# Optimization experiments

Measured on AMD Instinct MI355X. Metric: run time of the kernel, lower is better.

Reference implementation:

```python
import jax, jax.numpy as jnp
import numpy as np

# Model dims
B, S, D = 2, 1024, 1024          # batch, seq, d_model
NH, HD = 16, 64                  # n_heads, head_dim
E, K, H = 8, 2, 4096             # num_experts, experts_per_token, expert hidden
EPS = 1e-6
ROPE_BASE = 10000.0


def rmsnorm(x, w):
    # RMSNorm: x * rsqrt(mean(x^2) + eps) * weight (no mean-centering, no bias)
    return x * jax.lax.rsqrt(jnp.mean(x * x, axis=-1, keepdims=True) + EPS) * w


def apply_rope(q, k):
    # q,k: [B, NH, S, HD]; position_ids = arange(S) broadcast over batch
    hd = q.shape[-1]
    s = q.shape[2]
    inv_freq = 1.0 / (ROPE_BASE ** (jnp.arange(0, hd, 2, dtype=jnp.float32) / hd))
    freqs = jnp.arange(s, dtype=jnp.float32)[:, None] * inv_freq          # [S, HD/2]
    emb = jnp.concatenate([freqs, freqs], axis=-1)                        # [S, HD]
    cos = jnp.cos(emb)[None, None]                                        # [1,1,S,HD]
    sin = jnp.sin(emb)[None, None]

    def rotate_half(x):
        x1, x2 = jnp.split(x, 2, axis=-1)
        return jnp.concatenate([-x2, x1], axis=-1)

    return q * cos + rotate_half(q) * sin, k * cos + rotate_half(k) * sin


def setup_inputs() -> dict:
    key = jax.random.key(0)
    ks = jax.random.split(key, 9)
    sc = 0.02
    return {
        "x": jax.random.normal(ks[0], (B, S, D), jnp.float32),
        "attn_norm_w": jnp.ones((D,), jnp.float32),
        "wq": jax.random.normal(ks[1], (D, D), jnp.float32) * sc,
        "wk": jax.random.normal(ks[2], (D, D), jnp.float32) * sc,
        "wv": jax.random.normal(ks[3], (D, D), jnp.float32) * sc,
        "wo": jax.random.normal(ks[4], (D, D), jnp.float32) * sc,
        "moe_norm_w": jnp.ones((D,), jnp.float32),
        "gate_w": jax.random.normal(ks[5], (E, D), jnp.float32) * sc,
        "w1": jax.random.normal(ks[6], (E, H, D), jnp.float32) * sc,
        "b1": jnp.zeros((E, H), jnp.float32),
        "w2": jax.random.normal(ks[7], (E, D, H), jnp.float32) * sc,
        "b2": jnp.zeros((E, D), jnp.float32),
    }


def reference(x, attn_norm_w, wq, wk, wv, wo, moe_norm_w, gate_w, w1, b1, w2, b2):
    b, s, d = x.shape
    # --- pre-norm causal self-attention with RoPE (eval mode: no dropout) ---
    t = rmsnorm(x, attn_norm_w)
    q = (t @ wq.T).reshape(b, s, NH, HD).transpose(0, 2, 1, 3)
    k = (t @ wk.T).reshape(b, s, NH, HD).transpose(0, 2, 1, 3)
    v = (t @ wv.T).reshape(b, s, NH, HD).transpose(0, 2, 1, 3)
    q, k = apply_rope(q, k)
    scores = jnp.einsum("bhqd,bhkd->bhqk", q, k) / np.float32(np.sqrt(HD))
    causal = jnp.tril(jnp.ones((s, s), bool))
    scores = jnp.where(causal, scores, jnp.float32(-1e30))
    attn = jax.nn.softmax(scores, axis=-1)
    ao = jnp.einsum("bhqk,bhkd->bhqd", attn, v).transpose(0, 2, 1, 3).reshape(b, s, d)
    h = x + ao @ wo.T

    # --- sparse top-k MoE FFN (internal RMSNorm + residual) ---
    tn = rmsnorm(h, moe_norm_w).reshape(-1, d)                  # [T, D]
    logits = tn @ gate_w.T                                      # [T, E]
    gate_scores, idx = jax.lax.top_k(logits, K)                 # [T, K]
    rw = jax.nn.softmax(gate_scores, axis=-1)                   # [T, K]
    # compute all experts densely, then gather selected (same math as
    # gathering per-token expert weight matrices, far less memory traffic)
    hid = jax.nn.gelu(jnp.einsum("td,ehd->teh", tn, w1) + b1, approximate=False)
    eo = jnp.einsum("teh,edh->ted", hid, w2) + b2               # [T, E, D]
    sel = jnp.take_along_axis(eo, idx[:, :, None], axis=1)      # [T, K, D]
    moe_out = jnp.einsum("tkd,tk->td", sel, rw).reshape(b, s, d)
    return h + moe_out
```

## Files before the change

kernel.cpp:

```cpp
#include <hip/hip_runtime.h>
#include <hip/hip_bf16.h>
#include <hip/hip_fp16.h>


#define T_TOK 2048
#define DMODEL 1024
#define SEQ 1024
#define NEXP 8
#define HEXP 4096

typedef __attribute__((ext_vector_type(4))) float f32x4;
typedef __attribute__((ext_vector_type(4))) int i32x4;
typedef __attribute__((ext_vector_type(8))) short short8;
typedef __attribute__((ext_vector_type(8))) _Float16 half8;
typedef __attribute__((ext_vector_type(4))) _Float16 half4;

#define WAIT_VM3 asm volatile("s_waitcnt vmcnt(3)" ::: "memory")
#define WAIT_VM4 asm volatile("s_waitcnt vmcnt(4)" ::: "memory")
#define WAIT_VM6 asm volatile("s_waitcnt vmcnt(6)" ::: "memory")
#define WAIT_VM0 asm volatile("s_waitcnt vmcnt(0)" ::: "memory")
#define BARRIER __builtin_amdgcn_s_barrier()
#define SCHEDFENCE __builtin_amdgcn_sched_barrier(0)

__device__ __forceinline__ void gload16(const void* g, void* l)
{
    __builtin_amdgcn_global_load_lds((const __attribute__((address_space(1))) void*)g,
                                     (__attribute__((address_space(3))) void*)l, 16, 0, 0);
}

__device__ __forceinline__ void bsplit(float f, unsigned short& hi, unsigned short& lo)
{
    unsigned int u = __float_as_uint(f);
    unsigned int rh = (u + 0x7FFFu + ((u >> 16) & 1u)) >> 16;
    hi = (unsigned short)rh;
    float fl = f - __uint_as_float(rh << 16);
    unsigned int u2 = __float_as_uint(fl);
    lo = (unsigned short)((u2 + 0x7FFFu + ((u2 >> 16) & 1u)) >> 16);
}

__device__ __forceinline__ float gelu_fast(float v)
{
    float e = __expf(-1.5957691216f * v * (1.0f + 0.044715f * v * v));
    return v * __builtin_amdgcn_rcpf(1.0f + e);
}

__global__ __launch_bounds__(256) void cast2_f16_kernel(
    const float* __restrict__ s0, const float* __restrict__ s1,
    _Float16* __restrict__ d0, _Float16* __restrict__ d1, int n8)
{
    const float* src = blockIdx.y ? s1 : s0;
    _Float16* dst = blockIdx.y ? d1 : d0;
    int stride = gridDim.x * blockDim.x;
    for (int i = blockIdx.x * blockDim.x + threadIdx.x; i < n8; i += stride) {
        float4 a = ((const float4*)src)[2 * i];
        float4 b = ((const float4*)src)[2 * i + 1];
        half8 h = { (_Float16)a.x, (_Float16)a.y, (_Float16)a.z, (_Float16)a.w,
                    (_Float16)b.x, (_Float16)b.y, (_Float16)b.z, (_Float16)b.w };
        *(half8*)(dst + (size_t)i * 8) = h;
    }
}

__global__ __launch_bounds__(256) void split4_kernel(
    const float* __restrict__ s0, const float* __restrict__ s1,
    const float* __restrict__ s2, const float* __restrict__ s3,
    unsigned short* __restrict__ h0, unsigned short* __restrict__ h1,
    unsigned short* __restrict__ h2, unsigned short* __restrict__ h3,
    unsigned short* __restrict__ l0, unsigned short* __restrict__ l1,
    unsigned short* __restrict__ l2, unsigned short* __restrict__ l3, int n4)
{
    int z = blockIdx.y;
    const float* src = (z == 0) ? s0 : (z == 1) ? s1 : (z == 2) ? s2 : s3;
    unsigned short* hi = (z == 0) ? h0 : (z == 1) ? h1 : (z == 2) ? h2 : h3;
    unsigned short* lo = (z == 0) ? l0 : (z == 1) ? l1 : (z == 2) ? l2 : l3;
    int stride = gridDim.x * blockDim.x;
    for (int i = blockIdx.x * blockDim.x + threadIdx.x; i < n4; i += stride) {
        float4 v = ((const float4*)src)[i];
        ushort4 h, l;
        bsplit(v.x, h.x, l.x); bsplit(v.y, h.y, l.y);
        bsplit(v.z, h.z, l.z); bsplit(v.w, h.w, l.w);
        *(ushort4*)(hi + (size_t)i * 4) = h;
        *(ushort4*)(lo + (size_t)i * 4) = l;
    }
}

__global__ __launch_bounds__(256) void rmsnorm_kernel(const float* __restrict__ x,
                                                      const float* __restrict__ w,
                                                      float* __restrict__ of,
                                                      _Float16* __restrict__ oh,
                                                      unsigned short* __restrict__ ohi,
                                                      unsigned short* __restrict__ olo)
{
    int row = blockIdx.x;
    int t = threadIdx.x;
    float4 v = ((const float4*)(x + (size_t)row * DMODEL))[t];
    float ss = v.x * v.x + v.y * v.y + v.z * v.z + v.w * v.w;
#pragma unroll
    for (int off = 32; off > 0; off >>= 1) ss += __shfl_xor(ss, off);
    __shared__ float red[4];
    if ((t & 63) == 0) red[t >> 6] = ss;
    __syncthreads();
    float tot = red[0] + red[1] + red[2] + red[3];
    float sc = rsqrtf(tot * (1.0f / DMODEL) + 1e-6f);
    float4 w4 = ((const float4*)w)[t];
    float4 o;
    o.x = v.x * sc * w4.x; o.y = v.y * sc * w4.y; o.z = v.z * sc * w4.z; o.w = v.w * sc * w4.w;
    if (of) ((float4*)(of + (size_t)row * DMODEL))[t] = o;
    if (oh) {
        half4 h = { (_Float16)o.x, (_Float16)o.y, (_Float16)o.z, (_Float16)o.w };
        *(half4*)(oh + (size_t)row * DMODEL + t * 4) = h;
    }
    if (ohi) {
        ushort4 h, l;
        bsplit(o.x, h.x, l.x); bsplit(o.y, h.y, l.y);
        bsplit(o.z, h.z, l.z); bsplit(o.w, h.w, l.w);
        *(ushort4*)(ohi + (size_t)row * DMODEL + t * 4) = h;
        *(ushort4*)(olo + (size_t)row * DMODEL + t * 4) = l;
    }
}

__global__ __launch_bounds__(256) void gemm_split_kernel(
    const unsigned short* __restrict__ aH, const unsigned short* __restrict__ aL,
    const unsigned short* __restrict__ b0H, const unsigned short* __restrict__ b0L,
    const unsigned short* __restrict__ b1H, const unsigned short* __restrict__ b1L,
    const unsigned short* __restrict__ b2H, const unsigned short* __restrict__ b2L,
    float* __restrict__ C0, float* __restrict__ C1, float* __restrict__ C2,
    const float* __restrict__ resid, int K)
{
    const unsigned short* bH = (blockIdx.z == 0) ? b0H : (blockIdx.z == 1 ? b1H : b2H);
    const unsigned short* bL = (blockIdx.z == 0) ? b0L : (blockIdx.z == 1 ? b1L : b2L);
    float* C = (blockIdx.z == 0) ? C0 : (blockIdx.z == 1 ? C1 : C2);
    int m0 = blockIdx.y * 128, n0 = blockIdx.x * 64;
    __shared__ unsigned short AsH[2][128 * 32];
    __shared__ unsigned short AsL[2][128 * 32];
    __shared__ unsigned short BsH[2][64 * 32];
    __shared__ unsigned short BsL[2][64 * 32];
    int t = threadIdx.x, w = t >> 6, l = t & 63;
    int sa = l >> 2, sc = (l & 3) * 8;
    const unsigned short* gAH0 = aH + (size_t)(m0 + w * 32 + sa) * K + sc;
    const unsigned short* gAH1 = aH + (size_t)(m0 + w * 32 + 16 + sa) * K + sc;
    const unsigned short* gAL0 = aL + (size_t)(m0 + w * 32 + sa) * K + sc;
    const unsigned short* gAL1 = aL + (size_t)(m0 + w * 32 + 16 + sa) * K + sc;
    const unsigned short* gBH0 = bH + (size_t)(n0 + w * 16 + sa) * K + sc;
    const unsigned short* gBL0 = bL + (size_t)(n0 + w * 16 + sa) * K + sc;
    const int aoff0 = (w * 32) * 32;
    const int aoff1 = (w * 32 + 16) * 32;
    const int boff0 = (w * 16) * 32;
    int wr = w >> 1, wc = w & 1;
    f32x4 zero = { 0.0f, 0.0f, 0.0f, 0.0f };
    f32x4 acc[4][2];
#pragma unroll
    for (int i = 0; i < 4; i++)
#pragma unroll
        for (int j = 0; j < 2; j++) acc[i][j] = zero;

#define GS_STAGE(B, K0) do { \
    gload16(gAH0 + (K0), &AsH[B][aoff0]); gload16(gAH1 + (K0), &AsH[B][aoff1]); \
    gload16(gAL0 + (K0), &AsL[B][aoff0]); gload16(gAL1 + (K0), &AsL[B][aoff1]); \
    gload16(gBH0 + (K0), &BsH[B][boff0]); gload16(gBL0 + (K0), &BsL[B][boff0]); \
} while (0)

#define GS_COMPUTE(B) do { \
    short8 ah[4], al[4], bh8[2], bl8[2]; \
    _Pragma("unroll") \
    for (int mi = 0; mi < 4; mi++) { \
        int base = (wr * 64 + mi * 16 + (l & 15)) * 32 + (l >> 4) * 8; \
        ah[mi] = *(const short8*)&AsH[B][base]; \
        al[mi] = *(const short8*)&AsL[B][base]; } \
    _Pragma("unroll") \
    for (int ni = 0; ni < 2; ni++) { \
        int base = (wc * 32 + ni * 16 + (l & 15)) * 32 + (l >> 4) * 8; \
        bh8[ni] = *(const short8*)&BsH[B][base]; \
        bl8[ni] = *(const short8*)&BsL[B][base]; } \
    _Pragma("unroll") \
    for (int mi = 0; mi < 4; mi++) \
        _Pragma("unroll") \
        for (int ni = 0; ni < 2; ni++) { \
            acc[mi][ni] = __builtin_amdgcn_mfma_f32_16x16x32_bf16(ah[mi], bh8[ni], acc[mi][ni], 0, 0, 0); \
            acc[mi][ni] = __builtin_amdgcn_mfma_f32_16x16x32_bf16(ah[mi], bl8[ni], acc[mi][ni], 0, 0, 0); \
            acc[mi][ni] = __builtin_amdgcn_mfma_f32_16x16x32_bf16(al[mi], bh8[ni], acc[mi][ni], 0, 0, 0); } \
} while (0)

    const int nt = K >> 5;
    GS_STAGE(0, 0);
    for (int kt = 0; kt < nt; kt += 2) {
        GS_STAGE(1, (kt + 1) << 5);
        WAIT_VM6;
        BARRIER; SCHEDFENCE;
        GS_COMPUTE(0);
        BARRIER;
        if (kt + 2 < nt) {
            GS_STAGE(0, (kt + 2) << 5);
            WAIT_VM6;
        } else {
            WAIT_VM0;
        }
        BARRIER; SCHEDFENCE;
        GS_COMPUTE(1);
        BARRIER;
    }
#undef GS_STAGE
#undef GS_COMPUTE

#pragma unroll
    for (int mi = 0; mi < 4; mi++) {
#pragma unroll
        for (int r = 0; r < 4; r++) {
            int row = m0 + wr * 64 + mi * 16 + (l >> 4) * 4 + r;
#pragma unroll
            for (int ni = 0; ni < 2; ni++) {
                int col = n0 + wc * 32 + ni * 16 + (l & 15);
                float v = acc[mi][ni][r];
                if (resid) v += resid[(size_t)row * DMODEL + col];
                C[(size_t)row * DMODEL + col] = v;
            }
        }
    }
}

__global__ __launch_bounds__(256) void rope_split_kernel(
    const float* __restrict__ qf, const float* __restrict__ kf,
    unsigned short* __restrict__ qHi, unsigned short* __restrict__ qLo,
    unsigned short* __restrict__ kHi, unsigned short* __restrict__ kLo)
{
    int i = blockIdx.x * 256 + threadIdx.x;
    int tok = i >> 9;
    int r = i & 511;
    int hh = r >> 5, ii = r & 31;
    int s = tok & (SEQ - 1);
    int b = tok >> 10;
    float invf = powf(10000.0f, -(float)(2 * ii) * (1.0f / 64.0f));
    float ang = (float)s * invf;
    float c = cosf(ang), sn = sinf(ang);
    size_t base = (size_t)tok * DMODEL + hh * 64 + ii;
    float q1 = qf[base], q2 = qf[base + 32];
    float k1 = kf[base], k2 = kf[base + 32];
    float rq1 = (q1 * c - q2 * sn) * 0.125f;
    float rq2 = (q2 * c + q1 * sn) * 0.125f;
    float rk1 = k1 * c - k2 * sn;
    float rk2 = k2 * c + k1 * sn;
    int bh = b * 16 + hh;
    size_t qb = ((size_t)bh * SEQ + s) * 64 + ii;
    unsigned short h, lo;
    bsplit(rq1, h, lo); qHi[qb] = h; qLo[qb] = lo;
    bsplit(rq2, h, lo); qHi[qb + 32] = h; qLo[qb + 32] = lo;
    size_t kb = (size_t)bh * (SEQ * 64) + (size_t)(s >> 6) * 4096 + (size_t)(s & 63) * 64;
    int d1 = ii, d2 = ii + 32;
    int p1 = (((d1 >> 3) ^ (s & 7)) << 3) | (d1 & 7);
    int p2 = (((d2 >> 3) ^ (s & 7)) << 3) | (d2 & 7);
    bsplit(rk1, h, lo); kHi[kb + p1] = h; kLo[kb + p1] = lo;
    bsplit(rk2, h, lo); kHi[kb + p2] = h; kLo[kb + p2] = lo;
}

__global__ __launch_bounds__(256) void vtrans_kernel(const float* __restrict__ vf,
                                                     unsigned short* __restrict__ vtHi,
                                                     unsigned short* __restrict__ vtLo)
{
    int sb = blockIdx.x, bh = blockIdx.y;
    int b = bh >> 4, h = bh & 15;
    __shared__ unsigned short tH[64][72];
    __shared__ unsigned short tL[64][72];
    int t = threadIdx.x;
#pragma unroll
    for (int i = 0; i < 4; i++) {
        int idx = i * 256 + t, row = idx >> 4, c4 = idx & 15;
        float4 v = *(const float4*)(vf + (size_t)(b * SEQ + sb * 64 + row) * DMODEL + h * 64 + c4 * 4);
        unsigned short hh, ll;
        bsplit(v.x, hh, ll); tH[c4 * 4 + 0][row] = hh; tL[c4 * 4 + 0][row] = ll;
        bsplit(v.y, hh, ll); tH[c4 * 4 + 1][row] = hh; tL[c4 * 4 + 1][row] = ll;
        bsplit(v.z, hh, ll); tH[c4 * 4 + 2][row] = hh; tL[c4 * 4 + 2][row] = ll;
        bsplit(v.w, hh, ll); tH[c4 * 4 + 3][row] = hh; tL[c4 * 4 + 3][row] = ll;
    }
    __syncthreads();
#pragma unroll
    for (int i = 0; i < 4; i++) {
        int idx = i * 256 + t, d = idx >> 4, sc4 = idx & 15;
        ushort4 oh = { tH[d][sc4 * 4 + 0], tH[d][sc4 * 4 + 1], tH[d][sc4 * 4 + 2], tH[d][sc4 * 4 + 3] };
        ushort4 ol = { tL[d][sc4 * 4 + 0], tL[d][sc4 * 4 + 1], tL[d][sc4 * 4 + 2], tL[d][sc4 * 4 + 3] };
        size_t off = (size_t)bh * (64 * SEQ) + (size_t)sb * 4096 + (size_t)d * 64
                   + (((sc4 >> 1) ^ (d & 7)) << 3) + ((sc4 & 1) << 2);
        *(ushort4*)(vtHi + off) = oh;
        *(ushort4*)(vtLo + off) = ol;
    }
}

__global__ __launch_bounds__(512) void attn_mfma_kernel(
    const unsigned short* __restrict__ qHi, const unsigned short* __restrict__ qLo,
    const unsigned short* __restrict__ kHi, const unsigned short* __restrict__ kLo,
    const unsigned short* __restrict__ vtHi, const unsigned short* __restrict__ vtLo,
    float* __restrict__ Opart, float* __restrict__ mscr, float* __restrict__ lscr)
{
    int qt = 7 - blockIdx.x;
    int bh = blockIdx.y, ks = blockIdx.z;
    int t = threadIdx.x, w = t >> 6, l = t & 63;
    int lq = l & 15, g = l >> 4, lx = lq & 7;
    __shared__ unsigned short KsH[2][4096];
    __shared__ unsigned short KsL[2][4096];
    __shared__ unsigned short VsH[2][4096];
    __shared__ unsigned short VsL[2][4096];
    __shared__ unsigned short PsH[8][1024];
    __shared__ unsigned short PsL[8][1024];
    const size_t hb = (size_t)bh * (SEQ * 64);
    const unsigned short* kHp = kHi + hb;
    const unsigned short* kLp = kLo + hb;
    const unsigned short* vHp = vtHi + hb;
    const unsigned short* vLp = vtLo + hb;
    int qrow = qt * 128 + w * 16 + lq;
    short8 qh[2], qlo8[2];
#pragma unroll
    for (int c = 0; c < 2; c++) {
        size_t off = hb + (size_t)qrow * 64 + c * 32 + g * 8;
        qh[c]   = *(const short8*)(qHi + off);
        qlo8[c] = *(const short8*)(qLo + off);
    }
    f32x4 zero = { 0.0f, 0.0f, 0.0f, 0.0f };
    f32x4 acc_o[4];
#pragma unroll
    for (int i = 0; i < 4; i++) acc_o[i] = zero;
    float mrun = -3.0e38f, lrun = 0.0f;
    int ktl = ks ? (qt + 1) : 0;
    int kth = ks ? (2 * qt + 2) : (qt + 1);

#define AT_STAGE(B, KT) do { \
    size_t so = (size_t)(KT) * 4096 + (w * 64 + l) * 8; \
    gload16(kHp + so, &KsH[B][w * 512]); \
    gload16(kLp + so, &KsL[B][w * 512]); \
    gload16(vHp + so, &VsH[B][w * 512]); \
    gload16(vLp + so, &VsL[B][w * 512]); \
} while (0)

#define AT_COMPUTE(B, KT) do { \
    f32x4 sacc[4]; \
    _Pragma("unroll") \
    for (int i = 0; i < 4; i++) sacc[i] = zero; \
    _Pragma("unroll") \
    for (int nf = 0; nf < 4; nf++) { \
        _Pragma("unroll") \
        for (int c = 0; c < 2; c++) { \
            int ka = (nf * 16 + lq) * 64 + (((c * 4 + g) ^ lx) << 3); \
            short8 kh = *(const short8*)&KsH[B][ka]; \
            short8 kl = *(const short8*)&KsL[B][ka]; \
            sacc[nf] = __builtin_amdgcn_mfma_f32_16x16x32_bf16(kh, qh[c], sacc[nf], 0, 0, 0); \
            sacc[nf] = __builtin_amdgcn_mfma_f32_16x16x32_bf16(kh, qlo8[c], sacc[nf], 0, 0, 0); \
            sacc[nf] = __builtin_amdgcn_mfma_f32_16x16x32_bf16(kl, qh[c], sacc[nf], 0, 0, 0); \
        } \
    } \
    _Pragma("unroll") \
    for (int nf = 0; nf < 4; nf++) \
        _Pragma("unroll") \
        for (int r = 0; r < 4; r++) \
            if ((KT) * 64 + nf * 16 + g * 4 + r > qrow) sacc[nf][r] = -1.0e30f; \
    float mt = sacc[0][0]; \
    _Pragma("unroll") \
    for (int nf = 0; nf < 4; nf++) \
        _Pragma("unroll") \
        for (int r = 0; r < 4; r++) mt = fmaxf(mt, sacc[nf][r]); \
    mt = fmaxf(mt, __shfl_xor(mt, 16)); \
    mt = fmaxf(mt, __shfl_xor(mt, 32)); \
    float mnew = fmaxf(mrun, mt); \
    float p[4][4]; \
    float ps = 0.0f; \
    _Pragma("unroll") \
    for (int nf = 0; nf < 4; nf++) \
        _Pragma("unroll") \
        for (int r = 0; r < 4; r++) { \
            float e = __expf(sacc[nf][r] - mnew); \
            p[nf][r] = e; \
            ps += e; \
        } \
    ps += __shfl_xor(ps, 16); \
    ps += __shfl_xor(ps, 32); \
    float scale = __expf(mrun - mnew); \
    lrun = lrun * scale + ps; \
    mrun = mnew; \
    _Pragma("unroll") \
    for (int nf = 0; nf < 4; nf++) { \
        ushort4 ph, pl; \
        bsplit(p[nf][0], ph.x, pl.x); bsplit(p[nf][1], ph.y, pl.y); \
        bsplit(p[nf][2], ph.z, pl.z); bsplit(p[nf][3], ph.w, pl.w); \
        int pa = lq * 64 + (((nf * 2 + (g >> 1)) ^ lx) << 3) + ((g & 1) << 2); \
        *(ushort4*)&PsH[w][pa] = ph; \
        *(ushort4*)&PsL[w][pa] = pl; \
    } \
    float scq[4]; \
    _Pragma("unroll") \
    for (int r = 0; r < 4; r++) scq[r] = __shfl(scale, g * 4 + r); \
    _Pragma("unroll") \
    for (int df = 0; df < 4; df++) \
        _Pragma("unroll") \
        for (int r = 0; r < 4; r++) acc_o[df][r] *= scq[r]; \
    _Pragma("unroll") \
    for (int c = 0; c < 2; c++) { \
        int pa = lq * 64 + (((c * 4 + g) ^ lx) << 3); \
        short8 ph8 = *(const short8*)&PsH[w][pa]; \
        short8 pl8 = *(const short8*)&PsL[w][pa]; \
        _Pragma("unroll") \
        for (int df = 0; df < 4; df++) { \
            int va = (df * 16 + lq) * 64 + (((c * 4 + g) ^ lx) << 3); \
            short8 vh = *(const short8*)&VsH[B][va]; \
            short8 vl = *(const short8*)&VsL[B][va]; \
            acc_o[df] = __builtin_amdgcn_mfma_f32_16x16x32_bf16(ph8, vh, acc_o[df], 0, 0, 0); \
            acc_o[df] = __builtin_amdgcn_mfma_f32_16x16x32_bf16(ph8, vl, acc_o[df], 0, 0, 0); \
            acc_o[df] = __builtin_amdgcn_mfma_f32_16x16x32_bf16(pl8, vh, acc_o[df], 0, 0, 0); \
        } \
    } \
} while (0)

    int kt = ktl;
    AT_STAGE(0, kt);
    for (; kt + 1 < kth; kt += 2) {
        AT_STAGE(1, kt + 1);
        WAIT_VM4;
        BARRIER; SCHEDFENCE;
        AT_COMPUTE(0, kt);
        BARRIER;
        if (kt + 2 < kth) {
            AT_STAGE(0, kt + 2);
            WAIT_VM4;
        } else {
            WAIT_VM0;
        }
        BARRIER; SCHEDFENCE;
        AT_COMPUTE(1, kt + 1);
        BARRIER;
    }
    if (kt < kth) {
        WAIT_VM0;
        BARRIER; SCHEDFENCE;
        AT_COMPUTE(0, kt);
    }
#undef AT_STAGE
#undef AT_COMPUTE

    if (g == 0) {
        size_t mi = (size_t)(ks * 32 + bh) * SEQ + (size_t)(qt * 128 + w * 16 + lq);
        mscr[mi] = mrun;
        lscr[mi] = lrun;
    }
#pragma unroll
    for (int df = 0; df < 4; df++)
#pragma unroll
        for (int r = 0; r < 4; r++) {
            size_t row = (size_t)(ks * 32 + bh) * SEQ + (size_t)(qt * 128 + w * 16 + g * 4 + r);
            Opart[row * 64 + df * 16 + lq] = acc_o[df][r];
        }
}

__global__ __launch_bounds__(256) void attn_combine_kernel(
    const float* __restrict__ Opart, const float* __restrict__ mscr,
    const float* __restrict__ lscr,
    unsigned short* __restrict__ aoHi, unsigned short* __restrict__ aoLo)
{
    int i = blockIdx.x * 256 + threadIdx.x;
    int d4 = i & 15;
    int qr = (i >> 4) & (SEQ - 1);
    int bh = i >> 14;
    int b = bh >> 4, h = bh & 15;
    size_t r0 = (size_t)bh * SEQ + qr;
    size_t r1 = (size_t)(32 + bh) * SEQ + qr;
    float m0 = mscr[r0], m1 = mscr[r1];
    float l0 = lscr[r0], l1 = lscr[r1];
    float m = fmaxf(m0, m1);
    float w0 = __expf(m0 - m), w1 = __expf(m1 - m);
    float dn = 1.0f / (w0 * l0 + w1 * l1);
    float4 o0 = *(const float4*)(Opart + r0 * 64 + d4 * 4);
    float4 o1 = *(const float4*)(Opart + r1 * 64 + d4 * 4);
    float4 o;
    o.x = (w0 * o0.x + w1 * o1.x) * dn;
    o.y = (w0 * o0.y + w1 * o1.y) * dn;
    o.z = (w0 * o0.z + w1 * o1.z) * dn;
    o.w = (w0 * o0.w + w1 * o1.w) * dn;
    ushort4 hs, ls;
    bsplit(o.x, hs.x, ls.x); bsplit(o.y, hs.y, ls.y);
    bsplit(o.z, hs.z, ls.z); bsplit(o.w, hs.w, ls.w);
    size_t base = (size_t)b * SEQ * DMODEL + (size_t)qr * DMODEL + h * 64 + d4 * 4;
    *(ushort4*)(aoHi + base) = hs;
    *(ushort4*)(aoLo + base) = ls;
}

__global__ __launch_bounds__(256) void gate_kernel(const float* __restrict__ tn2f,
                                                   const float* __restrict__ gw,
                                                   float* __restrict__ logits)
{
    int tok = blockIdx.x;
    int t = threadIdx.x, e = t >> 5, l32 = t & 31;
    const float* xr = tn2f + (size_t)tok * DMODEL;
    const float* gr = gw + (size_t)e * DMODEL;
    float s = 0.0f;
    for (int j = l32; j < DMODEL; j += 32) s += xr[j] * gr[j];
#pragma unroll
    for (int off = 16; off > 0; off >>= 1) s += __shfl_down(s, off, 32);
    if (l32 == 0) logits[tok * NEXP + e] = s;
}

__global__ void zero_kernel(int* p, int n)
{
    int i = blockIdx.x * blockDim.x + threadIdx.x;
    if (i < n) p[i] = 0;
}

__global__ void top2_kernel(const float* __restrict__ logits, float* __restrict__ rw,
                            int* __restrict__ cnt, int* __restrict__ entry)
{
    int t = blockIdx.x * blockDim.x + threadIdx.x;
    if (t >= T_TOK) return;
    float l[8];
#pragma unroll
    for (int e = 0; e < 8; e++) l[e] = logits[t * 8 + e];
    int e0 = 0;
#pragma unroll
    for (int e = 1; e < 8; e++) if (l[e] > l[e0]) e0 = e;
    int e1 = (e0 == 0) ? 1 : 0;
#pragma unroll
    for (int e = 0; e < 8; e++) if (e != e0 && l[e] > l[e1]) e1 = e;
    float ex = expf(l[e1] - l[e0]);
    float denom = 1.0f + ex;
    rw[t * 2 + 0] = 1.0f / denom;
    rw[t * 2 + 1] = ex / denom;
    int pos = atomicAdd(&cnt[e0], 1);
    entry[e0 * 2048 + pos] = t * 2;
    pos = atomicAdd(&cnt[e1], 1);
    entry[e1 * 2048 + pos] = t * 2 + 1;
}

__global__ void offs_kernel(const int* __restrict__ cnt, int* __restrict__ offs)
{
    if (threadIdx.x == 0) {
        int s = 0;
        for (int e = 0; e < 8; e++) { offs[e] = s; s += cnt[e]; }
    }
}

__global__ __launch_bounds__(256) void moe_gemm1_kernel(
    const _Float16* __restrict__ tn2h, const _Float16* __restrict__ w1h,
    const float* __restrict__ b1, const int* __restrict__ cnt, const int* __restrict__ offs,
    const int* __restrict__ entry, _Float16* __restrict__ hid)
{
    int e = blockIdx.z;
    int ne = cnt[e];
    int m0 = blockIdx.y * 128;
    if (m0 >= ne) return;
    int n0 = blockIdx.x * 128;
    __shared__ _Float16 As[2][128 * 32];
    __shared__ _Float16 Bs[2][128 * 32];
    int t = threadIdx.x, w = t >> 6, l = t & 63;
    int sa = l >> 2, sc = (l & 3) * 8;
    int g0 = entry[e * 2048 + min(m0 + w * 32 + sa, ne - 1)] >> 1;
    int g1 = entry[e * 2048 + min(m0 + w * 32 + 16 + sa, ne - 1)] >> 1;
    const _Float16* gA0 = tn2h + (size_t)g0 * DMODEL + sc;
    const _Float16* gA1 = tn2h + (size_t)g1 * DMODEL + sc;
    const _Float16* w1e = w1h + (size_t)e * HEXP * DMODEL;
    const _Float16* gB0 = w1e + (size_t)(n0 + w * 32 + sa) * DMODEL + sc;
    const _Float16* gB1 = w1e + (size_t)(n0 + w * 32 + 16 + sa) * DMODEL + sc;
    const int aoff0 = (w * 32) * 32, aoff1 = (w * 32 + 16) * 32;
    int wr = w >> 1, wc = w & 1;
    f32x4 zero = { 0.0f, 0.0f, 0.0f, 0.0f };
    f32x4 acc[4][4];
#pragma unroll
    for (int i = 0; i < 4; i++)
#pragma unroll
        for (int j = 0; j < 4; j++) acc[i][j] = zero;

#define M1_STAGE(B, K0) do { \
    gload16(gA0 + (K0), &As[B][aoff0]); gload16(gA1 + (K0), &As[B][aoff1]); \
    gload16(gB0 + (K0), &Bs[B][aoff0]); gload16(gB1 + (K0), &Bs[B][aoff1]); \
} while (0)

#define M1_COMPUTE(B) do { \
    half8 af[4], bfr[4]; \
    _Pragma("unroll") \
    for (int mi = 0; mi < 4; mi++) \
        af[mi] = *(const half8*)&As[B][(wr * 64 + mi * 16 + (l & 15)) * 32 + (l >> 4) * 8]; \
    _Pragma("unroll") \
    for (int ni = 0; ni < 4; ni++) \
        bfr[ni] = *(const half8*)&Bs[B][(wc * 64 + ni * 16 + (l & 15)) * 32 + (l >> 4) * 8]; \
    _Pragma("unroll") \
    for (int mi = 0; mi < 4; mi++) \
        _Pragma("unroll") \
        for (int ni = 0; ni < 4; ni++) \
            acc[mi][ni] = __builtin_amdgcn_mfma_f32_16x16x32_f16(af[mi], bfr[ni], acc[mi][ni], 0, 0, 0); \
} while (0)

    const int nt = DMODEL >> 5;
    M1_STAGE(0, 0);
    for (int kt = 0; kt < nt; kt += 2) {
        M1_STAGE(1, (kt + 1) << 5);
        WAIT_VM4;
        BARRIER; SCHEDFENCE;
        M1_COMPUTE(0);
        BARRIER;
        if (kt + 2 < nt) {
            M1_STAGE(0, (kt + 2) << 5);
            WAIT_VM4;
        } else {
            WAIT_VM0;
        }
        BARRIER; SCHEDFENCE;
        M1_COMPUTE(1);
        BARRIER;
    }
#undef M1_STAGE
#undef M1_COMPUTE

    int off_e = offs[e];
#pragma unroll
    for (int mi = 0; mi < 4; mi++) {
#pragma unroll
        for (int r = 0; r < 4; r++) {
            int row = m0 + wr * 64 + mi * 16 + (l >> 4) * 4 + r;
            if (row < ne) {
                size_t orow = (size_t)(off_e + row) * HEXP;
#pragma unroll
                for (int ni = 0; ni < 4; ni++) {
                    int cg = n0 + wc * 64 + ni * 16 + (l & 15);
                    float v = acc[mi][ni][r] + b1[e * HEXP + cg];
                    hid[orow + cg] = (_Float16)gelu_fast(v);
                }
            }
        }
    }
}

__global__ __launch_bounds__(512) void moe_gemm2_kernel(
    const _Float16* __restrict__ hid, const _Float16* __restrict__ w2h,
    const float* __restrict__ b2, const int* __restrict__ cnt, const int* __restrict__ offs,
    const int* __restrict__ entry,
    float* __restrict__ eoA, float* __restrict__ eoB,
    float* __restrict__ eoC, float* __restrict__ eoD)
{
    int bid = blockIdx.x;
    int e = bid & 7;
    int rest = bid >> 3;
    int n_i = rest & 7;
    int rest2 = rest >> 3;
    int ks = rest2 & 3;
    int m_i = rest2 >> 2;
    int ne = cnt[e];
    int m0 = m_i * 256;
    if (m0 >= ne) return;
    int n0 = n_i * 128;
    int kbase = ks * (HEXP / 4);
    float* eoP = (ks == 0) ? eoA : (ks == 1) ? eoB : (ks == 2) ? eoC : eoD;
    __shared__ _Float16 As[2][256 * 32];
    __shared__ _Float16 Bs[2][128 * 32];
    int t = threadIdx.x, w = t >> 6, l = t & 63;
    int off_e = offs[e];
    int sa = l >> 2, sc = (l & 3) * 8;
    int r0 = off_e + min(m0 + w * 32 + sa, ne - 1);
    int r1 = off_e + min(m0 + w * 32 + 16 + sa, ne - 1);
    const _Float16* gA0 = hid + (size_t)r0 * HEXP + kbase + sc;
    const _Float16* gA1 = hid + (size_t)r1 * HEXP + kbase + sc;
    const _Float16* w2e = w2h + (size_t)e * DMODEL * HEXP;
    const _Float16* gB0 = w2e + (size_t)(n0 + w * 16 + sa) * HEXP + kbase + sc;
    const int aoff0 = (w * 32) * 32, aoff1 = (w * 32 + 16) * 32;
    const int boff0 = (w * 16) * 32;
    int wr = w >> 1, wc = w & 1;
    f32x4 zero = { 0.0f, 0.0f, 0.0f, 0.0f };
    f32x4 acc[4][4];
#pragma unroll
    for (int i = 0; i < 4; i++)
#pragma unroll
        for (int j = 0; j < 4; j++) acc[i][j] = zero;

#define M2_STAGE(B, K0) do { \
    gload16(gA0 + (K0), &As[B][aoff0]); gload16(gA1 + (K0), &As[B][aoff1]); \
    gload16(gB0 + (K0), &Bs[B][boff0]); \
} while (0)

#define M2_COMPUTE(B) do { \
    half8 af[4], bfr[4]; \
    _Pragma("unroll") \
    for (int mi = 0; mi < 4; mi++) \
        af[mi] = *(const half8*)&As[B][(wr * 64 + mi * 16 + (l & 15)) * 32 + (l >> 4) * 8]; \
    _Pragma("unroll") \
    for (int ni = 0; ni < 4; ni++) \
        bfr[ni] = *(const half8*)&Bs[B][(wc * 64 + ni * 16 + (l & 15)) * 32 + (l >> 4) * 8]; \
    _Pragma("unroll") \
    for (int mi = 0; mi < 4; mi++) \
        _Pragma("unroll") \
        for (int ni = 0; ni < 4; ni++) \
            acc[mi][ni] = __builtin_amdgcn_mfma_f32_16x16x32_f16(af[mi], bfr[ni], acc[mi][ni], 0, 0, 0); \
} while (0)

    const int nt = (HEXP / 4) >> 5;
    M2_STAGE(0, 0);
    for (int kt = 0; kt < nt; kt += 2) {
        M2_STAGE(1, (kt + 1) << 5);
        WAIT_VM3;
        BARRIER; SCHEDFENCE;
        M2_COMPUTE(0);
        BARRIER;
        if (kt + 2 < nt) {
            M2_STAGE(0, (kt + 2) << 5);
            WAIT_VM3;
        } else {
            WAIT_VM0;
        }
        BARRIER; SCHEDFENCE;
        M2_COMPUTE(1);
        BARRIER;
    }
#undef M2_STAGE
#undef M2_COMPUTE

#pragma unroll
    for (int mi = 0; mi < 4; mi++) {
#pragma unroll
        for (int r = 0; r < 4; r++) {
            int row = m0 + wr * 64 + mi * 16 + (l >> 4) * 4 + r;
            if (row < ne) {
                int t2k = entry[e * 2048 + row];
#pragma unroll
                for (int ni = 0; ni < 4; ni++) {
                    int cg = n0 + wc * 64 + ni * 16 + (l & 15);
                    float v = acc[mi][ni][r];
                    if (ks == 0) v += b2[e * DMODEL + cg];
                    eoP[(size_t)t2k * DMODEL + cg] = v;
                }
            }
        }
    }
}

__global__ __launch_bounds__(256) void combine_kernel(const float* __restrict__ hf,
                                                      const float* __restrict__ eoA,
                                                      const float* __restrict__ eoB,
                                                      const float* __restrict__ eoC,
                                                      const float* __restrict__ eoD,
                                                      const float* __restrict__ rw,
                                                      float* __restrict__ out)
{
    int i = blockIdx.x * 256 + threadIdx.x;
    int tok = i >> 8;
    int d4 = i & 255;
    float4 hv = ((const float4*)hf)[i];
    float p0 = rw[tok * 2], p1 = rw[tok * 2 + 1];
    size_t i0 = (size_t)(tok * 2) * 256 + d4;
    size_t i1 = (size_t)(tok * 2 + 1) * 256 + d4;
    float4 a0 = ((const float4*)eoA)[i0];
    float4 b0 = ((const float4*)eoB)[i0];
    float4 c0 = ((const float4*)eoC)[i0];
    float4 d0 = ((const float4*)eoD)[i0];
    float4 a1 = ((const float4*)eoA)[i1];
    float4 b1 = ((const float4*)eoB)[i1];
    float4 c1 = ((const float4*)eoC)[i1];
    float4 d1 = ((const float4*)eoD)[i1];
    float4 o;
    o.x = hv.x + p0 * (a0.x + b0.x + c0.x + d0.x) + p1 * (a1.x + b1.x + c1.x + d1.x);
    o.y = hv.y + p0 * (a0.y + b0.y + c0.y + d0.y) + p1 * (a1.y + b1.y + c1.y + d1.y);
    o.z = hv.z + p0 * (a0.z + b0.z + c0.z + d0.z) + p1 * (a1.z + b1.z + c1.z + d1.z);
    o.w = hv.w + p0 * (a0.w + b0.w + c0.w + d0.w) + p1 * (a1.w + b1.w + c1.w + d1.w);
    ((float4*)out)[i] = o;
}

extern "C" void kernel_launch(void* const* d_in, const int* in_sizes, int n_in,
                              void* d_out, int out_size, void* d_ws, size_t ws_size,
                              hipStream_t stream)
{
    const float* x   = (const float*)d_in[0];
    const float* anw = (const float*)d_in[1];
    const float* wq  = (const float*)d_in[2];
    const float* wk  = (const float*)d_in[3];
    const float* wv  = (const float*)d_in[4];
    const float* wo  = (const float*)d_in[5];
    const float* mnw = (const float*)d_in[6];
    const float* gw  = (const float*)d_in[7];
    const float* w1  = (const float*)d_in[8];
    const float* b1  = (const float*)d_in[9];
    const float* w2  = (const float*)d_in[10];
    const float* b2  = (const float*)d_in[11];
    float* out = (float*)d_out;

    char* p = (char*)d_ws;
    auto alloc = [&](size_t bytes) { char* q = p; p += (bytes + 255) & ~(size_t)255; return q; };
    const size_t TD = (size_t)T_TOK * DMODEL;
    unsigned short* tnHi = (unsigned short*)alloc(TD * 2);
    unsigned short* tnLo = (unsigned short*)alloc(TD * 2);
    float*    qf   = (float*)alloc(TD * 4);
    float*    kf   = (float*)alloc(TD * 4);
    float*    vf   = (float*)alloc(TD * 4);
    unsigned short* qHi = (unsigned short*)alloc(TD * 2);
    unsigned short* qLo = (unsigned short*)alloc(TD * 2);
    unsigned short* kHi = (unsigned short*)alloc(TD * 2);
    unsigned short* kLo = (unsigned short*)alloc(TD * 2);
    float*    hf   = (float*)alloc(TD * 4);
    unsigned short* wqH = (unsigned short*)alloc((size_t)DMODEL * DMODEL * 2);
    unsigned short* wqL = (unsigned short*)alloc((size_t)DMODEL * DMODEL * 2);
    unsigned short* wkH = (unsigned short*)alloc((size_t)DMODEL * DMODEL * 2);
    unsigned short* wkL = (unsigned short*)alloc((size_t)DMODEL * DMODEL * 2);
    unsigned short* wvH = (unsigned short*)alloc((size_t)DMODEL * DMODEL * 2);
    unsigned short* wvL = (unsigned short*)alloc((size_t)DMODEL * DMODEL * 2);
    unsigned short* woH = (unsigned short*)alloc((size_t)DMODEL * DMODEL * 2);
    unsigned short* woL = (unsigned short*)alloc((size_t)DMODEL * DMODEL * 2);
    _Float16* w1h  = (_Float16*)alloc((size_t)NEXP * HEXP * DMODEL * 2);
    _Float16* w2h  = (_Float16*)alloc((size_t)NEXP * HEXP * DMODEL * 2);
    _Float16* hid  = (_Float16*)alloc((size_t)4096 * HEXP * 2);
    float*    logits = (float*)alloc((size_t)T_TOK * NEXP * 4);
    float*    rw   = (float*)alloc((size_t)T_TOK * 2 * 4);
    int*      cnt  = (int*)alloc(256);
    int*      offs = (int*)alloc(256);
    int*      entry = (int*)alloc((size_t)NEXP * 2048 * 4);
    float*    mscr = (float*)alloc((size_t)2 * 32 * SEQ * 4);
    float*    lscr = (float*)alloc((size_t)2 * 32 * SEQ * 4);
    (void)ws_size; (void)in_sizes; (void)n_in; (void)out_size;

    unsigned short* vtHi = (unsigned short*)qf;
    unsigned short* vtLo = (unsigned short*)qf + TD;
    float* tn2f = qf;
    unsigned short* aoHi = (unsigned short*)kf;
    unsigned short* aoLo = (unsigned short*)kf + TD;
    _Float16* tn2h = (_Float16*)vf;
    float* eoA = (float*)qHi;
    float* eoB = (float*)wqH;
    float* Opart = (float*)w1h;
    float* eoC = (float*)((char*)w1h + (size_t)32 * 1024 * 1024);
    float* eoD = (float*)((char*)w1h + (size_t)48 * 1024 * 1024);

    split4_kernel<<<dim3(512, 4), 256, 0, stream>>>(wq, wk, wv, wo,
        wqH, wkH, wvH, woH, wqL, wkL, wvL, woL, DMODEL * DMODEL / 4);

    rmsnorm_kernel<<<T_TOK, 256, 0, stream>>>(x, anw, nullptr, (_Float16*)nullptr, tnHi, tnLo);
    gemm_split_kernel<<<dim3(16, 16, 3), 256, 0, stream>>>(
        tnHi, tnLo, wqH, wqL, wkH, wkL, wvH, wvL, qf, kf, vf, nullptr, DMODEL);
    rope_split_kernel<<<4096, 256, 0, stream>>>(qf, kf, qHi, qLo, kHi, kLo);
    vtrans_kernel<<<dim3(16, 32), 256, 0, stream>>>(vf, vtHi, vtLo);
    attn_mfma_kernel<<<dim3(8, 32, 2), 512, 0, stream>>>(qHi, qLo, kHi, kLo, vtHi, vtLo,
                                                         Opart, mscr, lscr);
    attn_combine_kernel<<<2048, 256, 0, stream>>>(Opart, mscr, lscr, aoHi, aoLo);
    gemm_split_kernel<<<dim3(16, 16, 1), 256, 0, stream>>>(
        aoHi, aoLo, woH, woL, woH, woL, woH, woL, hf, hf, hf, x, DMODEL);

    cast2_f16_kernel<<<dim3(4096, 2), 256, 0, stream>>>(w1, w2, w1h, w2h,
                                                        NEXP * HEXP * DMODEL / 8);

    rmsnorm_kernel<<<T_TOK, 256, 0, stream>>>(hf, mnw, tn2f, tn2h, nullptr, nullptr);
    gate_kernel<<<T_TOK, 256, 0, stream>>>(tn2f, gw, logits);
    zero_kernel<<<1, 64, 0, stream>>>(cnt, 8);
    top2_kernel<<<8, 256, 0, stream>>>(logits, rw, cnt, entry);
    offs_kernel<<<1, 1, 0, stream>>>(cnt, offs);
    moe_gemm1_kernel<<<dim3(32, 16, 8), 256, 0, stream>>>(tn2h, w1h, b1, cnt, offs, entry, hid);
    moe_gemm2_kernel<<<2048, 512, 0, stream>>>(hid, w2h, b2, cnt, offs, entry,
                                               eoA, eoB, eoC, eoD);
    combine_kernel<<<2048, 256, 0, stream>>>(hf, eoA, eoB, eoC, eoD, rw, out);
}
```

Measured before the change: 428.5 us.

## Fuse expert weight cast into attention launch and retile MoE GEMM1 with swizzled LDS

```diff
diff --git a/kernel.cpp b/kernel.cpp
--- a/kernel.cpp
+++ b/kernel.cpp
@@ -42,22 +42,6 @@
 {
     float e = __expf(-1.5957691216f * v * (1.0f + 0.044715f * v * v));
     return v * __builtin_amdgcn_rcpf(1.0f + e);
-}
-
-__global__ __launch_bounds__(256) void cast2_f16_kernel(
-    const float* __restrict__ s0, const float* __restrict__ s1,
-    _Float16* __restrict__ d0, _Float16* __restrict__ d1, int n8)
-{
-    const float* src = blockIdx.y ? s1 : s0;
-    _Float16* dst = blockIdx.y ? d1 : d0;
-    int stride = gridDim.x * blockDim.x;
-    for (int i = blockIdx.x * blockDim.x + threadIdx.x; i < n8; i += stride) {
-        float4 a = ((const float4*)src)[2 * i];
-        float4 b = ((const float4*)src)[2 * i + 1];
-        half8 h = { (_Float16)a.x, (_Float16)a.y, (_Float16)a.z, (_Float16)a.w,
-                    (_Float16)b.x, (_Float16)b.y, (_Float16)b.z, (_Float16)b.w };
-        *(half8*)(dst + (size_t)i * 8) = h;
-    }
 }
 
 __global__ __launch_bounds__(256) void split4_kernel(
@@ -283,14 +267,34 @@
     }
 }
 
-__global__ __launch_bounds__(512) void attn_mfma_kernel(
+__global__ __launch_bounds__(512) void attn_cast_kernel(
     const unsigned short* __restrict__ qHi, const unsigned short* __restrict__ qLo,
     const unsigned short* __restrict__ kHi, const unsigned short* __restrict__ kLo,
     const unsigned short* __restrict__ vtHi, const unsigned short* __restrict__ vtLo,
-    float* __restrict__ Opart, float* __restrict__ mscr, float* __restrict__ lscr)
-{
-    int qt = 7 - blockIdx.x;
-    int bh = blockIdx.y, ks = blockIdx.z;
+    float* __restrict__ Opart, float* __restrict__ mscr, float* __restrict__ lscr,
+    const float* __restrict__ w1f, const float* __restrict__ w2f,
+    _Float16* __restrict__ w1h, _Float16* __restrict__ w2h)
+{
+    int bid = blockIdx.x;
+    if (bid >= 512) {
+        int cb = bid - 512;
+        const float* src = w1f;
+        _Float16* dst = w1h;
+        if (cb >= 512) { src = w2f; dst = w2h; cb -= 512; }
+        const int n8 = NEXP * HEXP * DMODEL / 8;
+        const int stride = 512 * 512;
+        for (int i = cb * 512 + threadIdx.x; i < n8; i += stride) {
+            float4 a = ((const float4*)src)[2 * i];
+            float4 b = ((const float4*)src)[2 * i + 1];
+            half8 h = { (_Float16)a.x, (_Float16)a.y, (_Float16)a.z, (_Float16)a.w,
+                        (_Float16)b.x, (_Float16)b.y, (_Float16)b.z, (_Float16)b.w };
+            *(half8*)(dst + (size_t)i * 8) = h;
+        }
+        return;
+    }
+    int qt = 7 - (bid & 7);
+    int bh = (bid >> 3) & 31;
+    int ks = bid >> 8;
     int t = threadIdx.x, w = t >> 6, l = t & 63;
     int lq = l & 15, g = l >> 4, lx = lq & 7;
     __shared__ unsigned short KsH[2][4096];
@@ -530,28 +534,34 @@
     }
 }
 
-__global__ __launch_bounds__(256) void moe_gemm1_kernel(
+__global__ __launch_bounds__(512) void moe_gemm1_kernel(
     const _Float16* __restrict__ tn2h, const _Float16* __restrict__ w1h,
     const float* __restrict__ b1, const int* __restrict__ cnt, const int* __restrict__ offs,
     const int* __restrict__ entry, _Float16* __restrict__ hid)
 {
-    int e = blockIdx.z;
+    int bid = blockIdx.x;
+    int e = bid & 7;
+    int n_i = (bid >> 3) & 31;
+    int m_i = bid >> 8;
     int ne = cnt[e];
-    int m0 = blockIdx.y * 128;
+    int m0 = m_i * 256;
     if (m0 >= ne) return;
-    int n0 = blockIdx.x * 128;
-    __shared__ _Float16 As[2][128 * 32];
+    int n0 = n_i * 128;
+    __shared__ _Float16 As[2][256 * 32];
     __shared__ _Float16 Bs[2][128 * 32];
     int t = threadIdx.x, w = t >> 6, l = t & 63;
-    int sa = l >> 2, sc = (l & 3) * 8;
+    int sa = l >> 2;
+    int swz = (l >> 3) & 3;
+    int scA = ((l & 3) ^ swz) * 8;
+    int rcol = ((l >> 4) ^ ((l >> 1) & 3)) * 8;
     int g0 = entry[e * 2048 + min(m0 + w * 32 + sa, ne - 1)] >> 1;
     int g1 = entry[e * 2048 + min(m0 + w * 32 + 16 + sa, ne - 1)] >> 1;
-    const _Float16* gA0 = tn2h + (size_t)g0 * DMODEL + sc;
-    const _Float16* gA1 = tn2h + (size_t)g1 * DMODEL + sc;
+    const _Float16* gA0 = tn2h + (size_t)g0 * DMODEL + scA;
+    const _Float16* gA1 = tn2h + (size_t)g1 * DMODEL + scA;
     const _Float16* w1e = w1h + (size_t)e * HEXP * DMODEL;
-    const _Float16* gB0 = w1e + (size_t)(n0 + w * 32 + sa) * DMODEL + sc;
-    const _Float16* gB1 = w1e + (size_t)(n0 + w * 32 + 16 + sa) * DMODEL + sc;
+    const _Float16* gB0 = w1e + (size_t)(n0 + w * 16 + sa) * DMODEL + scA;
     const int aoff0 = (w * 32) * 32, aoff1 = (w * 32 + 16) * 32;
+    const int boff0 = (w * 16) * 32;
     int wr = w >> 1, wc = w & 1;
     f32x4 zero = { 0.0f, 0.0f, 0.0f, 0.0f };
     f32x4 acc[4][4];
@@ -562,17 +572,17 @@
 
 #define M1_STAGE(B, K0) do { \
     gload16(gA0 + (K0), &As[B][aoff0]); gload16(gA1 + (K0), &As[B][aoff1]); \
-    gload16(gB0 + (K0), &Bs[B][aoff0]); gload16(gB1 + (K0), &Bs[B][aoff1]); \
+    gload16(gB0 + (K0), &Bs[B][boff0]); \
 } while (0)
 
 #define M1_COMPUTE(B) do { \
     half8 af[4], bfr[4]; \
     _Pragma("unroll") \
     for (int mi = 0; mi < 4; mi++) \
-        af[mi] = *(const half8*)&As[B][(wr * 64 + mi * 16 + (l & 15)) * 32 + (l >> 4) * 8]; \
+        af[mi] = *(const half8*)&As[B][(wr * 64 + mi * 16 + (l & 15)) * 32 + rcol]; \
     _Pragma("unroll") \
     for (int ni = 0; ni < 4; ni++) \
-        bfr[ni] = *(const half8*)&Bs[B][(wc * 64 + ni * 16 + (l & 15)) * 32 + (l >> 4) * 8]; \
+        bfr[ni] = *(const half8*)&Bs[B][(wc * 64 + ni * 16 + (l & 15)) * 32 + rcol]; \
     _Pragma("unroll") \
     for (int mi = 0; mi < 4; mi++) \
         _Pragma("unroll") \
@@ -584,13 +594,13 @@
     M1_STAGE(0, 0);
     for (int kt = 0; kt < nt; kt += 2) {
         M1_STAGE(1, (kt + 1) << 5);
-        WAIT_VM4;
+        WAIT_VM3;
         BARRIER; SCHEDFENCE;
         M1_COMPUTE(0);
         BARRIER;
         if (kt + 2 < nt) {
             M1_STAGE(0, (kt + 2) << 5);
-            WAIT_VM4;
+            WAIT_VM3;
         } else {
             WAIT_VM0;
         }
@@ -644,13 +654,16 @@
     __shared__ _Float16 Bs[2][128 * 32];
     int t = threadIdx.x, w = t >> 6, l = t & 63;
     int off_e = offs[e];
-    int sa = l >> 2, sc = (l & 3) * 8;
+    int sa = l >> 2;
+    int swz = (l >> 3) & 3;
+    int scA = ((l & 3) ^ swz) * 8;
+    int rcol = ((l >> 4) ^ ((l >> 1) & 3)) * 8;
     int r0 = off_e + min(m0 + w * 32 + sa, ne - 1);
     int r1 = off_e + min(m0 + w * 32 + 16 + sa, ne - 1);
-    const _Float16* gA0 = hid + (size_t)r0 * HEXP + kbase + sc;
-    const _Float16* gA1 = hid + (size_t)r1 * HEXP + kbase + sc;
+    const _Float16* gA0 = hid + (size_t)r0 * HEXP + kbase + scA;
+    const _Float16* gA1 = hid + (size_t)r1 * HEXP + kbase + scA;
     const _Float16* w2e = w2h + (size_t)e * DMODEL * HEXP;
-    const _Float16* gB0 = w2e + (size_t)(n0 + w * 16 + sa) * HEXP + kbase + sc;
+    const _Float16* gB0 = w2e + (size_t)(n0 + w * 16 + sa) * HEXP + kbase + scA;
     const int aoff0 = (w * 32) * 32, aoff1 = (w * 32 + 16) * 32;
     const int boff0 = (w * 16) * 32;
     int wr = w >> 1, wc = w & 1;
@@ -670,10 +683,10 @@
     half8 af[4], bfr[4]; \
     _Pragma("unroll") \
     for (int mi = 0; mi < 4; mi++) \
-        af[mi] = *(const half8*)&As[B][(wr * 64 + mi * 16 + (l & 15)) * 32 + (l >> 4) * 8]; \
+        af[mi] = *(const half8*)&As[B][(wr * 64 + mi * 16 + (l & 15)) * 32 + rcol]; \
     _Pragma("unroll") \
     for (int ni = 0; ni < 4; ni++) \
-        bfr[ni] = *(const half8*)&Bs[B][(wc * 64 + ni * 16 + (l & 15)) * 32 + (l >> 4) * 8]; \
+        bfr[ni] = *(const half8*)&Bs[B][(wc * 64 + ni * 16 + (l & 15)) * 32 + rcol]; \
     _Pragma("unroll") \
     for (int mi = 0; mi < 4; mi++) \
         _Pragma("unroll") \
@@ -811,7 +824,7 @@
     _Float16* tn2h = (_Float16*)vf;
     float* eoA = (float*)qHi;
     float* eoB = (float*)wqH;
-    float* Opart = (float*)w1h;
+    float* Opart = (float*)hid;
     float* eoC = (float*)((char*)w1h + (size_t)32 * 1024 * 1024);
     float* eoD = (float*)((char*)w1h + (size_t)48 * 1024 * 1024);
 
@@ -823,21 +836,18 @@
         tnHi, tnLo, wqH, wqL, wkH, wkL, wvH, wvL, qf, kf, vf, nullptr, DMODEL);
     rope_split_kernel<<<4096, 256, 0, stream>>>(qf, kf, qHi, qLo, kHi, kLo);
     vtrans_kernel<<<dim3(16, 32), 256, 0, stream>>>(vf, vtHi, vtLo);
-    attn_mfma_kernel<<<dim3(8, 32, 2), 512, 0, stream>>>(qHi, qLo, kHi, kLo, vtHi, vtLo,
-                                                         Opart, mscr, lscr);
+    attn_cast_kernel<<<1536, 512, 0, stream>>>(qHi, qLo, kHi, kLo, vtHi, vtLo,
+                                               Opart, mscr, lscr, w1, w2, w1h, w2h);
     attn_combine_kernel<<<2048, 256, 0, stream>>>(Opart, mscr, lscr, aoHi, aoLo);
     gemm_split_kernel<<<dim3(16, 16, 1), 256, 0, stream>>>(
         aoHi, aoLo, woH, woL, woH, woL, woH, woL, hf, hf, hf, x, DMODEL);
-
-    cast2_f16_kernel<<<dim3(4096, 2), 256, 0, stream>>>(w1, w2, w1h, w2h,
-                                                        NEXP * HEXP * DMODEL / 8);
 
     rmsnorm_kernel<<<T_TOK, 256, 0, stream>>>(hf, mnw, tn2f, tn2h, nullptr, nullptr);
     gate_kernel<<<T_TOK, 256, 0, stream>>>(tn2f, gw, logits);
     zero_kernel<<<1, 64, 0, stream>>>(cnt, 8);
     top2_kernel<<<8, 256, 0, stream>>>(logits, rw, cnt, entry);
     offs_kernel<<<1, 1, 0, stream>>>(cnt, offs);
-    moe_gemm1_kernel<<<dim3(32, 16, 8), 256, 0, stream>>>(tn2h, w1h, b1, cnt, offs, entry, hid);
+    moe_gemm1_kernel<<<2048, 512, 0, stream>>>(tn2h, w1h, b1, cnt, offs, entry, hid);
     moe_gemm2_kernel<<<2048, 512, 0, stream>>>(hid, w2h, b2, cnt, offs, entry,
                                                eoA, eoB, eoC, eoD);
     combine_kernel<<<2048, 256, 0, stream>>>(hf, eoA, eoB, eoC, eoD, rw, out);
```

Result: faster. 418.8 us (-2.3%).
